# Kernel optimization log

Measured on AMD Instinct MI355X. Metric: run time of the kernel, lower is better.

Reference implementation:

```python
import jax, jax.numpy as jnp
import numpy as np

N = 4096        # batch nodes
E = 65536       # random edges (self-loops appended -> 69632 total)
F_IN = 256
H = 128
C = 2
MIN = 1024      # minority (class 1) count; first MIN nodes
REP = 2         # int(N_pct/100) synthetic reps per minority sample


def setup_inputs() -> dict:
    key = jax.random.key(0)
    ks = jax.random.split(key, 24)
    feat = jax.random.normal(ks[0], (N, F_IN), dtype=jnp.float32)
    src = jax.random.randint(ks[1], (E,), 0, N, dtype=jnp.int32)
    dst = jax.random.randint(ks[2], (E,), 0, N, dtype=jnp.int32)
    loops = jnp.arange(N, dtype=jnp.int32)
    src = jnp.concatenate([src, loops])
    dst = jnp.concatenate([dst, loops])
    # dense batch adjacency (target for EdgeLoss), A[i,j]=1 if edge j->i
    adj = jnp.zeros((N, N), dtype=jnp.float32).at[dst, src].set(1.0)
    # deterministic labels: first MIN nodes are minority class 1
    labels = jnp.concatenate([jnp.ones((MIN,), jnp.int32), jnp.zeros((N - MIN,), jnp.int32)])

    def w(k, shape, fan_in):
        return jax.random.normal(k, shape, dtype=jnp.float32) / np.sqrt(fan_in)

    params = dict(
        W_pool0=w(ks[3], (F_IN, F_IN), F_IN), b_pool0=jnp.zeros((F_IN,), jnp.float32),
        W_self0=w(ks[4], (H, F_IN), F_IN), W_neigh0=w(ks[5], (H, F_IN), F_IN), b0=jnp.zeros((H,), jnp.float32),
        W_pool1=w(ks[6], (H, H), H), b_pool1=jnp.zeros((H,), jnp.float32),
        W_self1=w(ks[7], (H, H), H), W_neigh1=w(ks[8], (H, H), H), b1=jnp.zeros((H,), jnp.float32),
        de_weight=jax.random.uniform(ks[9], (H, H), jnp.float32, -1.0 / np.sqrt(H), 1.0 / np.sqrt(H)),
        W_conv=w(ks[10], (H, 2 * H), 2 * H),
        W_clf=w(ks[11], (C, H), H), b_clf=jnp.zeros((C,), jnp.float32),
        gaps=jax.random.uniform(ks[12], (MIN, REP), jnp.float32),  # SMOTE interpolation gaps
    )
    return dict(feat=feat, adj=adj, src=src, dst=dst, labels=labels, **params)


def _sage_pool_layer(h, src, dst, W_pool, b_pool, W_self, W_neigh, b):
    # DGL SAGEConv aggregator_type='pool': max over neighbors of relu(fc_pool(h))
    p = jax.nn.relu(h @ W_pool.T + b_pool)                     # [N, d]
    hn = jax.ops.segment_max(p[src], dst, num_segments=h.shape[0])
    hn = jnp.where(jnp.isfinite(hn), hn, 0.0)
    return h @ W_self.T + hn @ W_neigh.T + b


def _l2norm(x, eps=1e-12):
    return x / jnp.maximum(jnp.linalg.norm(x, axis=1, keepdims=True), eps)


def _smote_nn_interp(cand, gaps):
    # pairwise euclidean distances (vectorized form of the per-row loop)
    sq = jnp.sum(cand * cand, axis=1)
    d2 = sq[:, None] + sq[None, :] - 2.0 * (cand @ cand.T)
    dist = jnp.sqrt(jnp.maximum(d2, 0.0))
    nn_idx = jnp.argsort(dist, axis=1)[:, 1]                   # k=2 -> single nearest (excl. self)
    diff = cand[nn_idx] - cand                                  # [MIN, H]
    synth = cand[:, None, :] + gaps[:, :, None] * diff[:, None, :]  # [MIN, REP, H], i-major order
    return synth.reshape(MIN * REP, cand.shape[1])


def reference(feat, adj, src, dst, labels,
              W_pool0, b_pool0, W_self0, W_neigh0, b0,
              W_pool1, b_pool1, W_self1, W_neigh1, b1,
              de_weight, W_conv, W_clf, b_clf, gaps):
    # ---- Encoder (2 SAGEConv 'pool' layers; dropout is eval-mode identity) ----
    h = _sage_pool_layer(feat, src, dst, W_pool0, b_pool0, W_self0, W_neigh0, b0)
    h = _l2norm(jax.nn.relu(h))
    h = _sage_pool_layer(h, src, dst, W_pool1, b_pool1, W_self1, W_neigh1, b1)
    # ---- SMOTE (minority = first MIN rows, by deterministic label construction) ----
    synth = _smote_nn_interp(h[:MIN], gaps)
    x = jnp.concatenate([h, synth], axis=0)                    # [N + MIN*REP, H]
    y = jnp.concatenate([labels, jnp.ones((MIN * REP,), jnp.int32)])
    # ---- Decoder: sigmoid(out @ out.T) ----
    out = x @ de_weight.T
    pred_adj = jax.nn.sigmoid(out @ out.T)                     # [6144, 6144]
    # ---- EdgeLoss vs dense batch adjacency ----
    rec = pred_adj[:N, :N]
    edge_num = jnp.sum(adj != 0).astype(jnp.float32)
    neg_w = edge_num / (float(N * N) - edge_num)
    weight = jnp.where(adj == 0, neg_w, 1.0)
    loss = jnp.sum(weight * (rec - adj) ** 2)
    # ---- threshold + SageClassifier (1 layer, no activation before clf) ----
    pred_adj = jnp.where(pred_adj >= 0.5, pred_adj, 0.0)
    neigh = (pred_adj @ x) / (jnp.sum(pred_adj, axis=1, keepdims=True) + 1.0)
    hc = jnp.concatenate([x, neigh], axis=-1) @ W_conv.T
    logits = hc @ W_clf.T + b_clf                              # [6144, 2]
    return logits, y, loss
```

## Files before the change

kernel.cpp:

```cpp
#include <hip/hip_runtime.h>
#include <cstddef>

typedef unsigned short ushort_t;
typedef __attribute__((ext_vector_type(8))) short bf16x8;
typedef __attribute__((ext_vector_type(4))) float f32x4;
typedef __attribute__((ext_vector_type(16))) float f32x16;

#define WS_P0     0u
#define WS_DOTS   0u
#define WS_OBK    524288u
#define WS_HN0    1048576u
#define WS_H1     2097152u
#define WS_H1N    2621440u
#define WS_P1     3145728u
#define WS_PVB    3145728u
#define WS_HN1    3670016u
#define WS_H2     4194304u
#define WS_X      4718592u
#define WS_BITMAP 5767168u
#define WS_NEIGH  6291456u
#define WS_ROWSUM 7077888u
#define WS_SCAL   7084032u
#define WS_DEG    7084048u
#define WS_NN     7088144u
#define WS_CUR    7089168u
#define WS_ROWPTR 7093264u
#define WS_EIDX   7097361u

__device__ inline ushort_t f2bf(float f) {
  unsigned u = __float_as_uint(f);
  u += 0x7fff + ((u >> 16) & 1);
  return (ushort_t)(u >> 16);
}
__device__ inline float bf2f(ushort_t h) {
  return __uint_as_float((unsigned)h << 16);
}

__global__ __launch_bounds__(256, 2) void mgemm(
    const float* __restrict__ A, int lda,
    const float* __restrict__ B, int ldb,
    const float* __restrict__ A2, int lda2,
    const float* __restrict__ B2, int ldb2,
    const float* __restrict__ bias,
    float* __restrict__ C, int ldc,
    int K, int relu,
    ushort_t* __restrict__ Cb,
    const float* __restrict__ a2scale,
    const float* __restrict__ Ahi,
    const float* __restrict__ Wclf,
    const float* __restrict__ scal4,
    float* __restrict__ outp)
{
  __shared__ ushort_t AhS[64][36], AlS[64][36], BhS[64][36], BlS[64][36];
  const int tid = threadIdx.x;
  const int lane = tid & 63;
  const int w = tid >> 6;
  const int lo = lane & 31, hi = lane >> 5;
  const int iq = (w & 1) << 5, jq = (w >> 1) << 5;
  const int i0 = blockIdx.y << 6, j0 = blockIdx.x << 6;
  const int lr = tid >> 2;
  const int c8 = (tid & 3) << 3;
  f32x16 acc;
#pragma unroll
  for (int t = 0; t < 16; ++t) acc[t] = 0.f;
  const int npass = (A2 != nullptr) ? 2 : 1;
  for (int pass = 0; pass < npass; ++pass) {
    const float* Ap = pass ? A2 : A; const int la = pass ? lda2 : lda;
    const float* Bp = pass ? B2 : B; const int lb = pass ? ldb2 : ldb;
    const float* Arow = (pass == 0 && Ahi != nullptr && (i0 + lr) >= 4096)
        ? (Ahi + (size_t)(i0 + lr - 4096) * la)
        : (Ap + (size_t)(i0 + lr) * la);
    const float* Brow = Bp + (size_t)(j0 + lr) * lb;
    const float sc = (pass && a2scale) ? __frcp_rn(a2scale[i0 + lr] + 1.f) : 1.f;
    for (int k0 = 0; k0 < K; k0 += 32) {
      float av[8], bv[8];
      {
        const float4 a0 = *(const float4*)(Arow + k0 + c8);
        const float4 a1 = *(const float4*)(Arow + k0 + c8 + 4);
        const float4 b0 = *(const float4*)(Brow + k0 + c8);
        const float4 b1 = *(const float4*)(Brow + k0 + c8 + 4);
        av[0]=a0.x*sc; av[1]=a0.y*sc; av[2]=a0.z*sc; av[3]=a0.w*sc;
        av[4]=a1.x*sc; av[5]=a1.y*sc; av[6]=a1.z*sc; av[7]=a1.w*sc;
        bv[0]=b0.x; bv[1]=b0.y; bv[2]=b0.z; bv[3]=b0.w;
        bv[4]=b1.x; bv[5]=b1.y; bv[6]=b1.z; bv[7]=b1.w;
      }
      __syncthreads();
      {
        ushort_t ah8[8], al8[8], bh8[8], bl8[8];
#pragma unroll
        for (int e = 0; e < 8; ++e) {
          const ushort_t ah = f2bf(av[e]);
          ah8[e] = ah; al8[e] = f2bf(av[e] - bf2f(ah));
          const ushort_t bh = f2bf(bv[e]);
          bh8[e] = bh; bl8[e] = f2bf(bv[e] - bf2f(bh));
        }
        *(bf16x8*)&AhS[lr][c8] = *(bf16x8*)ah8;
        *(bf16x8*)&AlS[lr][c8] = *(bf16x8*)al8;
        *(bf16x8*)&BhS[lr][c8] = *(bf16x8*)bh8;
        *(bf16x8*)&BlS[lr][c8] = *(bf16x8*)bl8;
      }
      __syncthreads();
#pragma unroll
      for (int kk = 0; kk < 32; kk += 16) {
        const bf16x8 ahf = *(const bf16x8*)&AhS[iq + lo][kk + (hi << 3)];
        const bf16x8 alf = *(const bf16x8*)&AlS[iq + lo][kk + (hi << 3)];
        const bf16x8 bhf = *(const bf16x8*)&BhS[jq + lo][kk + (hi << 3)];
        const bf16x8 blf = *(const bf16x8*)&BlS[jq + lo][kk + (hi << 3)];
        acc = __builtin_amdgcn_mfma_f32_32x32x16_bf16(ahf, bhf, acc, 0, 0, 0);
        acc = __builtin_amdgcn_mfma_f32_32x32x16_bf16(alf, bhf, acc, 0, 0, 0);
        acc = __builtin_amdgcn_mfma_f32_32x32x16_bf16(ahf, blf, acc, 0, 0, 0);
      }
    }
  }
  const int col = j0 + jq + lo;
  if (Wclf) {
    const float w0c = Wclf[col], w1c = Wclf[128 + col];
#pragma unroll
    for (int t = 0; t < 16; ++t) {
      float q0 = acc[t] * w0c, q1 = acc[t] * w1c;
#pragma unroll
      for (int m = 1; m < 32; m <<= 1) {
        q0 += __shfl_xor(q0, m, 64);
        q1 += __shfl_xor(q1, m, 64);
      }
      if (lo == 0) {
        const int row = i0 + iq + (t & 3) + ((t >> 2) << 3) + (hi << 2);
        atomicAdd(&outp[(size_t)row * 2 + 0], q0);
        atomicAdd(&outp[(size_t)row * 2 + 1], q1);
      }
    }
    if (blockIdx.x == 0 && blockIdx.y == 0 && tid == 0) {
      const float cnt = scal4[4];
      const float neg_w = cnt / (16777216.f - cnt);
      outp[18432] = neg_w * (scal4[0] - scal4[3]) + scal4[1];
    }
    return;
  }
  const float badd = bias ? bias[col] : 0.f;
#pragma unroll
  for (int t = 0; t < 16; ++t) {
    float o = acc[t] + badd;
    if (relu) o = fmaxf(o, 0.f);
    const int row = i0 + iq + (t & 3) + ((t >> 2) << 3) + (hi << 2);
    if (Cb) {
      const size_t off = ((size_t)(row >> 5) << 12) +
          (size_t)(((col >> 4) << 9) +
                   (((((col >> 3) & 1) << 5) + (row & 31)) << 3) + (col & 7));
      Cb[off] = f2bf(o);
    } else {
      C[(size_t)row * ldc + col] = o;
    }
  }
}

__global__ void count_bitmap_k(const int* __restrict__ src, const int* __restrict__ dst,
                               int* __restrict__ deg, unsigned* __restrict__ bitmap, int E) {
  const int e = blockIdx.x * 256 + threadIdx.x;
  if (e < E) {
    const int d_ = dst[e], s_ = src[e];
    atomicAdd(&deg[d_], 1);
    const unsigned cell = ((unsigned)d_ << 12) + (unsigned)s_;
    atomicOr(&bitmap[cell >> 5], 1u << (cell & 31));
  }
}

__global__ __launch_bounds__(1024) void scan_k(const int* __restrict__ deg,
                                               int* __restrict__ rowptr,
                                               int* __restrict__ cursor) {
  __shared__ int sums[1024];
  const int t = threadIdx.x;
  const int4 d = *(const int4*)(deg + (t << 2));
  const int local = d.x + d.y + d.z + d.w;
  sums[t] = local;
  __syncthreads();
  for (int off = 1; off < 1024; off <<= 1) {
    int v = (t >= off) ? sums[t - off] : 0;
    __syncthreads();
    sums[t] += v;
    __syncthreads();
  }
  const int excl = sums[t] - local;
  const int o0 = excl, o1 = o0 + d.x, o2 = o1 + d.y, o3 = o2 + d.z;
  rowptr[(t<<2)+0]=o0; rowptr[(t<<2)+1]=o1; rowptr[(t<<2)+2]=o2; rowptr[(t<<2)+3]=o3;
  cursor[(t<<2)+0]=o0; cursor[(t<<2)+1]=o1; cursor[(t<<2)+2]=o2; cursor[(t<<2)+3]=o3;
  if (t == 1023) rowptr[4096] = sums[1023];
}

__global__ void fill_k(const int* __restrict__ src, const int* __restrict__ dst,
                       int* __restrict__ cursor, int* __restrict__ eidx, int E) {
  const int e = blockIdx.x * 256 + threadIdx.x;
  if (e < E) {
    const int p = atomicAdd(&cursor[dst[e]], 1);
    eidx[p] = src[e];
  }
}

__global__ void segmax_k(const float* __restrict__ p, const int* __restrict__ rowptr,
                         const int* __restrict__ eidx, float* __restrict__ hn, int F) {
  const int row = blockIdx.x, f = threadIdx.x;
  const int b = rowptr[row], e = rowptr[row + 1];
  float m0 = 0.f, m1 = 0.f;
  int k = b;
  for (; k + 1 < e; k += 2) {
    m0 = fmaxf(m0, p[(size_t)eidx[k] * F + f]);
    m1 = fmaxf(m1, p[(size_t)eidx[k + 1] * F + f]);
  }
  if (k < e) m0 = fmaxf(m0, p[(size_t)eidx[k] * F + f]);
  hn[(size_t)row * F + f] = fmaxf(m0, m1);
}

__device__ inline float wave_sum(float v) {
#pragma unroll
  for (int o = 32; o > 0; o >>= 1) v += __shfl_down(v, o, 64);
  return v;
}

__global__ void relu_l2norm_k(const float* __restrict__ in, float* __restrict__ out) {
  const int row = blockIdx.x, f = threadIdx.x;
  const float v = fmaxf(in[(size_t)row * 128 + f], 0.f);
  const float ss = wave_sum(v * v);
  __shared__ float w[2];
  if ((f & 63) == 0) w[f >> 6] = ss;
  __syncthreads();
  const float denom = fmaxf(sqrtf(w[0] + w[1]), 1e-12f);
  out[(size_t)row * 128 + f] = v / denom;
}

__global__ void argmin_k(const float* __restrict__ dots, int* __restrict__ nn) {
  __shared__ float sqd[1024];
  const int i = blockIdx.x, tid = threadIdx.x;
#pragma unroll
  for (int z = 0; z < 4; ++z) {
    const int j = (tid << 2) + z;
    sqd[j] = dots[(size_t)j * 1025];
  }
  __syncthreads();
  float best = 3.402823466e38f; int bidx = 0x7fffffff;
  const float si = sqd[i];
  for (int j = tid; j < 1024; j += 256) {
    if (j == i) continue;
    float d2 = si + sqd[j] - 2.f * dots[(size_t)i * 1024 + j];
    d2 = fmaxf(d2, 0.f);
    if (d2 < best || (d2 == best && j < bidx)) { best = d2; bidx = j; }
  }
  __shared__ float bv[256]; __shared__ int bi[256];
  bv[tid] = best; bi[tid] = bidx;
  __syncthreads();
  for (int s = 128; s > 0; s >>= 1) {
    if (tid < s) {
      if (bv[tid+s] < bv[tid] || (bv[tid+s] == bv[tid] && bi[tid+s] < bi[tid])) {
        bv[tid] = bv[tid+s]; bi[tid] = bi[tid+s];
      }
    }
    __syncthreads();
  }
  if (tid == 0) nn[i] = bi[0];
}

__global__ __launch_bounds__(256) void build_pack_k(
    const float* __restrict__ h2, const int* __restrict__ nn,
    const float* __restrict__ gaps, float* __restrict__ synth,
    ushort_t* __restrict__ pvb,
    const int* __restrict__ labels, const float* __restrict__ bclf,
    float* __restrict__ outp) {
  __shared__ ushort_t s[4096];
  const int jt = blockIdx.x, tid = threadIdx.x;
  if (tid < 32) {
    const int i = (jt << 5) + tid;
    outp[(size_t)i * 2 + 0] = bclf[0];
    outp[(size_t)i * 2 + 1] = bclf[1];
    outp[12288 + i] = (i < 4096) ? (float)labels[i] : 1.f;
  }
  if (jt < 128) {
    const float* ip = h2 + ((size_t)jt << 12);
#pragma unroll
    for (int k = 0; k < 4; ++k) {
      const float4 v = *(const float4*)(ip + (tid << 4) + (k << 2));
      ushort4 h; h.x = f2bf(v.x); h.y = f2bf(v.y); h.z = f2bf(v.z); h.w = f2bf(v.w);
      *(ushort4*)(s + (tid << 4) + (k << 2)) = h;
    }
  } else {
    const int row = tid >> 3;
    const int sIdx = ((jt - 128) << 5) + row;
    const int i = sIdx >> 1;
    const float g = gaps[sIdx];
    const int ni = nn[i];
#pragma unroll
    for (int k = 0; k < 4; ++k) {
      const int f = ((tid & 7) << 4) + (k << 2);
      const float4 c4 = *(const float4*)(h2 + (size_t)i * 128 + f);
      const float4 n4 = *(const float4*)(h2 + (size_t)ni * 128 + f);
      float4 v;
      v.x = c4.x + g * (n4.x - c4.x);
      v.y = c4.y + g * (n4.y - c4.y);
      v.z = c4.z + g * (n4.z - c4.z);
      v.w = c4.w + g * (n4.w - c4.w);
      *(float4*)(synth + (size_t)sIdx * 128 + f) = v;
      ushort4 h; h.x = f2bf(v.x); h.y = f2bf(v.y); h.z = f2bf(v.z); h.w = f2bf(v.w);
      *(ushort4*)(s + (row << 7) + f) = h;
    }
  }
  __syncthreads();
  const int u = tid & 31, ft = (tid >> 5) & 3, cc = tid >> 7;
  ushort_t* op = pvb + ((size_t)jt << 12) + (cc << 11) + (ft << 9);
#pragma unroll
  for (int m = 0; m < 2; ++m) {
    const int l = (u << 1) + m;
    const int f = (ft << 5) + (l & 31);
    const int jb = (cc << 4) + ((l >> 5) << 3);
    ushort4 o0, o1;
    o0.x = s[(jb + 0) * 128 + f]; o0.y = s[(jb + 1) * 128 + f];
    o0.z = s[(jb + 2) * 128 + f]; o0.w = s[(jb + 3) * 128 + f];
    o1.x = s[(jb + 4) * 128 + f]; o1.y = s[(jb + 5) * 128 + f];
    o1.z = s[(jb + 6) * 128 + f]; o1.w = s[(jb + 7) * 128 + f];
    *(ushort4*)(op + (l << 3) + 0) = o0;
    *(ushort4*)(op + (l << 3) + 4) = o1;
  }
}

__global__ __launch_bounds__(256, 2) void fused_mfma(
    const ushort_t* __restrict__ obk,
    const ushort_t* __restrict__ pvb,
    const unsigned* __restrict__ bitmap,
    float* __restrict__ neigh,
    float* __restrict__ rowsum,
    float* __restrict__ scal)
{
  __shared__ float wred[4][4];
  const int tid = threadIdx.x;
  const int w = tid >> 6;
  const int lane = tid & 63;
  const int lo = lane & 31, hi = lane >> 5;
  const int it = (blockIdx.x << 2) + w;
  const int iw = it << 5;
  const int jt0 = blockIdx.y * 24;
  const bool loss_i = (it < 128);

  bf16x8 qf[8];
  {
    const ushort_t* qp = obk + ((size_t)it << 12) + (lane << 3);
#pragma unroll
    for (int c = 0; c < 8; ++c) qf[c] = *(const bf16x8*)(qp + (c << 9));
  }
  f32x16 oacc[4];
#pragma unroll
  for (int ft = 0; ft < 4; ++ft)
#pragma unroll
    for (int r = 0; r < 16; ++r) oacc[ft][r] = 0.f;
  float rs = 0.f, s_all = 0.f, s1a = 0.f, suba = 0.f, ecf = 0.f;

  bf16x8 a[8];
  {
    const ushort_t* kp = obk + ((size_t)jt0 << 12) + (lane << 3);
#pragma unroll
    for (int c = 0; c < 8; ++c) a[c] = *(const bf16x8*)(kp + (c << 9));
  }

  for (int t = 0; t < 24; ++t) {
    const int jt = jt0 + t;
    f32x16 s0, s1;
#pragma unroll
    for (int r = 0; r < 16; ++r) { s0[r] = 0.f; s1[r] = 0.f; }
    __builtin_amdgcn_s_setprio(1);
#pragma unroll
    for (int c = 0; c < 4; ++c) {
      s0 = __builtin_amdgcn_mfma_f32_32x32x16_bf16(a[c], qf[c], s0, 0, 0, 0);
      s1 = __builtin_amdgcn_mfma_f32_32x32x16_bf16(a[c + 4], qf[c + 4], s1, 0, 0, 0);
    }
    __builtin_amdgcn_s_setprio(0);
    bf16x8 bvf[2][4];
    {
      const ushort_t* vp = pvb + ((size_t)jt << 12) + (lane << 3);
#pragma unroll
      for (int cc = 0; cc < 2; ++cc)
#pragma unroll
        for (int ft = 0; ft < 4; ++ft)
          bvf[cc][ft] = *(const bf16x8*)(vp + (cc << 11) + (ft << 9));
    }
    if (t < 23) {
      const ushort_t* kp = obk + ((size_t)(jt + 1) << 12) + (lane << 3);
#pragma unroll
      for (int c = 0; c < 8; ++c) a[c] = *(const bf16x8*)(kp + (c << 9));
    }
    const bool loss_t = loss_i && (jt < 128);
    unsigned word = 0u;
    if (loss_t) word = bitmap[((unsigned)(iw + lo) << 7) + (unsigned)jt];
    float p[16];
    if (loss_t) {
      ecf += (float)__popc(word & (0x0F0F0F0Fu << (hi << 2)));
#pragma unroll
      for (int r = 0; r < 16; ++r) {
        const float v = s0[r] + s1[r];
        const float sg = __builtin_amdgcn_rcpf(1.f + __expf(-v));
        const int jl = (r & 3) + ((r >> 2) << 3) + (hi << 2);
        const float e_ = (float)((word >> jl) & 1u);
        s_all += sg * sg;
        s1a  += e_ * (sg - 1.f) * (sg - 1.f);
        suba += e_ * sg * sg;
        const float tv = (v >= 0.f) ? sg : 0.f;
        p[r] = tv; rs += tv;
      }
    } else {
#pragma unroll
      for (int r = 0; r < 16; ++r) {
        const float v = s0[r] + s1[r];
        const float sg = __builtin_amdgcn_rcpf(1.f + __expf(-v));
        const float tv = (v >= 0.f) ? sg : 0.f;
        p[r] = tv; rs += tv;
      }
    }
#pragma unroll
    for (int cc = 0; cc < 2; ++cc) {
      const int b8 = cc << 3;
      unsigned c01, c23, c45, c67;
      asm("v_cvt_pk_bf16_f32 %0, %1, %2" : "=v"(c01) : "v"(p[b8+0]), "v"(p[b8+1]));
      asm("v_cvt_pk_bf16_f32 %0, %1, %2" : "=v"(c23) : "v"(p[b8+2]), "v"(p[b8+3]));
      asm("v_cvt_pk_bf16_f32 %0, %1, %2" : "=v"(c45) : "v"(p[b8+4]), "v"(p[b8+5]));
      asm("v_cvt_pk_bf16_f32 %0, %1, %2" : "=v"(c67) : "v"(p[b8+6]), "v"(p[b8+7]));
      const auto w0 = __builtin_amdgcn_permlane32_swap((int)c01, (int)c45, false, false);
      const auto w1 = __builtin_amdgcn_permlane32_swap((int)c23, (int)c67, false, false);
      union { int i[4]; bf16x8 h; } u;
      u.i[0] = w0[0]; u.i[1] = w1[0]; u.i[2] = w0[1]; u.i[3] = w1[1];
      __builtin_amdgcn_s_setprio(1);
#pragma unroll
      for (int ft = 0; ft < 4; ++ft)
        oacc[ft] = __builtin_amdgcn_mfma_f32_32x32x16_bf16(u.h, bvf[cc][ft], oacc[ft], 0, 0, 0);
      __builtin_amdgcn_s_setprio(0);
    }
  }
#pragma unroll
  for (int ft = 0; ft < 4; ++ft)
#pragma unroll
    for (int r = 0; r < 16; ++r) {
      const int ir = (r & 3) + ((r >> 2) << 3) + (hi << 2);
      atomicAdd(&neigh[(size_t)(iw + ir) * 128 + (ft << 5) + lo], oacc[ft][r]);
    }
  rs += __shfl_xor(rs, 32, 64);
  if (hi == 0) atomicAdd(&rowsum[iw + lo], rs);
  {
    float v0 = wave_sum(s_all), v1 = wave_sum(s1a), v2 = wave_sum(suba), v3 = wave_sum(ecf);
    if (lane == 0) { wred[w][0] = v0; wred[w][1] = v1; wred[w][2] = v2; wred[w][3] = v3; }
  }
  __syncthreads();
  if (tid < 4) {
    const float t = wred[0][tid] + wred[1][tid] + wred[2][tid] + wred[3][tid];
    const int dst = (tid == 0) ? 0 : (tid == 1) ? 1 : (tid == 2) ? 3 : 4;
    atomicAdd(&scal[dst], t);
  }
}

extern "C" void kernel_launch(void* const* d_in, const int* in_sizes, int n_in,
                              void* d_out, int out_size, void* d_ws, size_t ws_size,
                              hipStream_t stream) {
  const float* feat     = (const float*)d_in[0];
  const int*   src      = (const int*)d_in[2];
  const int*   dst      = (const int*)d_in[3];
  const int*   labels   = (const int*)d_in[4];
  const float* W_pool0  = (const float*)d_in[5];
  const float* b_pool0  = (const float*)d_in[6];
  const float* W_self0  = (const float*)d_in[7];
  const float* W_neigh0 = (const float*)d_in[8];
  const float* b0       = (const float*)d_in[9];
  const float* W_pool1  = (const float*)d_in[10];
  const float* b_pool1  = (const float*)d_in[11];
  const float* W_self1  = (const float*)d_in[12];
  const float* W_neigh1 = (const float*)d_in[13];
  const float* b1       = (const float*)d_in[14];
  const float* de_w     = (const float*)d_in[15];
  const float* W_conv   = (const float*)d_in[16];
  const float* W_clf    = (const float*)d_in[17];
  const float* b_clf    = (const float*)d_in[18];
  const float* gaps     = (const float*)d_in[19];
  const int E = in_sizes[2];

  float* ws = (float*)d_ws;
  float* p0       = ws + WS_P0;
  float* dots     = ws + WS_DOTS;
  ushort_t* obk   = (ushort_t*)(ws + WS_OBK);
  float* hn0      = ws + WS_HN0;
  unsigned* bitmap= (unsigned*)(ws + WS_BITMAP);
  float* h1       = ws + WS_H1;
  float* h1n      = ws + WS_H1N;
  float* p1       = ws + WS_P1;
  ushort_t* pvb   = (ushort_t*)(ws + WS_PVB);
  float* hn1      = ws + WS_HN1;
  float* h2       = ws + WS_H2;
  float* synth    = ws + WS_X;
  float* neigh    = ws + WS_NEIGH;
  float* rowsum   = ws + WS_ROWSUM;
  float* scal     = ws + WS_SCAL;
  int* deg        = (int*)(ws + WS_DEG);
  int* nn         = (int*)(ws + WS_NN);
  int* cursor     = (int*)(ws + WS_CUR);
  int* rowptr     = (int*)(ws + WS_ROWPTR);
  int* eidx       = (int*)(ws + WS_EIDX);

  float* outp = (float*)d_out;
  const dim3 blk(256);

  hipMemsetAsync(bitmap, 0, (size_t)(WS_DEG + 4096 - WS_BITMAP) * 4, stream);

  count_bitmap_k<<<(E + 255) / 256, blk, 0, stream>>>(src, dst, deg, bitmap, E);
  scan_k<<<1, 1024, 0, stream>>>(deg, rowptr, cursor);
  fill_k<<<(E + 255) / 256, blk, 0, stream>>>(src, dst, cursor, eidx, E);

  mgemm<<<dim3(4, 64), blk, 0, stream>>>(feat, 256, W_pool0, 256,
                                         nullptr, 0, nullptr, 0,
                                         b_pool0, p0, 256, 256, 1, nullptr, nullptr, nullptr,
                                         nullptr, nullptr, nullptr);
  segmax_k<<<4096, 256, 0, stream>>>(p0, rowptr, eidx, hn0, 256);
  mgemm<<<dim3(2, 64), blk, 0, stream>>>(feat, 256, W_self0, 256,
                                         hn0, 256, W_neigh0, 256,
                                         b0, h1, 128, 256, 0, nullptr, nullptr, nullptr,
                                         nullptr, nullptr, nullptr);
  relu_l2norm_k<<<4096, 128, 0, stream>>>(h1, h1n);

  mgemm<<<dim3(2, 64), blk, 0, stream>>>(h1n, 128, W_pool1, 128,
                                         nullptr, 0, nullptr, 0,
                                         b_pool1, p1, 128, 128, 1, nullptr, nullptr, nullptr,
                                         nullptr, nullptr, nullptr);
  segmax_k<<<4096, 128, 0, stream>>>(p1, rowptr, eidx, hn1, 128);
  mgemm<<<dim3(2, 64), blk, 0, stream>>>(h1n, 128, W_self1, 128,
                                         hn1, 128, W_neigh1, 128,
                                         b1, h2, 128, 128, 0, nullptr, nullptr, nullptr,
                                         nullptr, nullptr, nullptr);

  mgemm<<<dim3(16, 16), blk, 0, stream>>>(h2, 128, h2, 128,
                                          nullptr, 0, nullptr, 0,
                                          nullptr, dots, 1024, 128, 0, nullptr, nullptr, nullptr,
                                          nullptr, nullptr, nullptr);
  argmin_k<<<1024, 256, 0, stream>>>(dots, nn);
  build_pack_k<<<192, blk, 0, stream>>>(h2, nn, gaps, synth, pvb, labels, b_clf, outp);

  mgemm<<<dim3(2, 96), blk, 0, stream>>>(h2, 128, de_w, 128,
                                         nullptr, 0, nullptr, 0,
                                         nullptr, nullptr, 0, 128, 0, obk, nullptr, synth,
                                         nullptr, nullptr, nullptr);
  fused_mfma<<<dim3(48, 8), blk, 0, stream>>>(obk, pvb, bitmap, neigh, rowsum, scal);

  mgemm<<<dim3(2, 96), blk, 0, stream>>>(h2, 128, W_conv, 256,
                                         neigh, 128, W_conv + 128, 256,
                                         nullptr, nullptr, 128, 128, 0, nullptr, rowsum, synth,
                                         W_clf, scal, outp);

  (void)n_in; (void)out_size; (void)ws_size; (void)in_sizes;
}
```

Before: 296.9 us.

## Raise fused_mfma occupancy by splitting j-range and trimming register footprint

Doubles the y-grid of the fused decoder/aggregation kernel so each block covers 12 column tiles instead of 24, and raises the launch-bounds occupancy target from 2 to 3 blocks per CU. Register pressure drops because the next-tile K prefetch is removed, the two split score accumulators become a single chained MFMA accumulator, and the V fragments are loaded per half instead of all at once. The cost is more atomic adds into neigh/rowsum from twice as many blocks, no software prefetch, and a serial dependency chain across the eight score MFMAs.

```diff
diff --git a/kernel.cpp b/kernel.cpp
--- a/kernel.cpp
+++ b/kernel.cpp
@@ -318,7 +318,7 @@
   }
 }
 
-__global__ __launch_bounds__(256, 2) void fused_mfma(
+__global__ __launch_bounds__(256, 3) void fused_mfma(
     const ushort_t* __restrict__ obk,
     const ushort_t* __restrict__ pvb,
     const unsigned* __restrict__ bitmap,
@@ -333,7 +333,7 @@
   const int lo = lane & 31, hi = lane >> 5;
   const int it = (blockIdx.x << 2) + w;
   const int iw = it << 5;
-  const int jt0 = blockIdx.y * 24;
+  const int jt0 = blockIdx.y * 12;
   const bool loss_i = (it < 128);
 
   bf16x8 qf[8];
@@ -349,74 +349,64 @@
     for (int r = 0; r < 16; ++r) oacc[ft][r] = 0.f;
   float rs = 0.f, s_all = 0.f, s1a = 0.f, suba = 0.f, ecf = 0.f;
 
-  bf16x8 a[8];
-  {
-    const ushort_t* kp = obk + ((size_t)jt0 << 12) + (lane << 3);
-#pragma unroll
-    for (int c = 0; c < 8; ++c) a[c] = *(const bf16x8*)(kp + (c << 9));
-  }
-
-  for (int t = 0; t < 24; ++t) {
+  for (int t = 0; t < 12; ++t) {
     const int jt = jt0 + t;
-    f32x16 s0, s1;
-#pragma unroll
-    for (int r = 0; r < 16; ++r) { s0[r] = 0.f; s1[r] = 0.f; }
-    __builtin_amdgcn_s_setprio(1);
-#pragma unroll
-    for (int c = 0; c < 4; ++c) {
-      s0 = __builtin_amdgcn_mfma_f32_32x32x16_bf16(a[c], qf[c], s0, 0, 0, 0);
-      s1 = __builtin_amdgcn_mfma_f32_32x32x16_bf16(a[c + 4], qf[c + 4], s1, 0, 0, 0);
-    }
-    __builtin_amdgcn_s_setprio(0);
-    bf16x8 bvf[2][4];
+    bf16x8 a[8];
     {
-      const ushort_t* vp = pvb + ((size_t)jt << 12) + (lane << 3);
-#pragma unroll
-      for (int cc = 0; cc < 2; ++cc)
-#pragma unroll
-        for (int ft = 0; ft < 4; ++ft)
-          bvf[cc][ft] = *(const bf16x8*)(vp + (cc << 11) + (ft << 9));
-    }
-    if (t < 23) {
-      const ushort_t* kp = obk + ((size_t)(jt + 1) << 12) + (lane << 3);
+      const ushort_t* kp = obk + ((size_t)jt << 12) + (lane << 3);
 #pragma unroll
       for (int c = 0; c < 8; ++c) a[c] = *(const bf16x8*)(kp + (c << 9));
     }
     const bool loss_t = loss_i && (jt < 128);
     unsigned word = 0u;
     if (loss_t) word = bitmap[((unsigned)(iw + lo) << 7) + (unsigned)jt];
-    float p[16];
-    if (loss_t) {
-      ecf += (float)__popc(word & (0x0F0F0F0Fu << (hi << 2)));
-#pragma unroll
-      for (int r = 0; r < 16; ++r) {
-        const float v = s0[r] + s1[r];
-        const float sg = __builtin_amdgcn_rcpf(1.f + __expf(-v));
-        const int jl = (r & 3) + ((r >> 2) << 3) + (hi << 2);
-        const float e_ = (float)((word >> jl) & 1u);
-        s_all += sg * sg;
-        s1a  += e_ * (sg - 1.f) * (sg - 1.f);
-        suba += e_ * sg * sg;
-        const float tv = (v >= 0.f) ? sg : 0.f;
-        p[r] = tv; rs += tv;
-      }
-    } else {
-#pragma unroll
-      for (int r = 0; r < 16; ++r) {
-        const float v = s0[r] + s1[r];
-        const float sg = __builtin_amdgcn_rcpf(1.f + __expf(-v));
-        const float tv = (v >= 0.f) ? sg : 0.f;
-        p[r] = tv; rs += tv;
-      }
-    }
+    f32x16 s;
+#pragma unroll
+    for (int r = 0; r < 16; ++r) s[r] = 0.f;
+    __builtin_amdgcn_s_setprio(1);
+#pragma unroll
+    for (int c = 0; c < 8; ++c)
+      s = __builtin_amdgcn_mfma_f32_32x32x16_bf16(a[c], qf[c], s, 0, 0, 0);
+    __builtin_amdgcn_s_setprio(0);
+    if (loss_t) ecf += (float)__popc(word & (0x0F0F0F0Fu << (hi << 2)));
 #pragma unroll
     for (int cc = 0; cc < 2; ++cc) {
-      const int b8 = cc << 3;
+      bf16x8 bvf[4];
+      {
+        const ushort_t* vp = pvb + ((size_t)jt << 12) + (cc << 11) + (lane << 3);
+#pragma unroll
+        for (int ft = 0; ft < 4; ++ft)
+          bvf[ft] = *(const bf16x8*)(vp + (ft << 9));
+      }
+      float p8[8];
+      if (loss_t) {
+#pragma unroll
+        for (int rr = 0; rr < 8; ++rr) {
+          const int r = (cc << 3) + rr;
+          const float v = s[r];
+          const float sg = __builtin_amdgcn_rcpf(1.f + __expf(-v));
+          const int jl = (r & 3) + ((r >> 2) << 3) + (hi << 2);
+          const float e_ = (float)((word >> jl) & 1u);
+          s_all += sg * sg;
+          s1a  += e_ * (sg - 1.f) * (sg - 1.f);
+          suba += e_ * sg * sg;
+          const float tv = (v >= 0.f) ? sg : 0.f;
+          p8[rr] = tv; rs += tv;
+        }
+      } else {
+#pragma unroll
+        for (int rr = 0; rr < 8; ++rr) {
+          const float v = s[(cc << 3) + rr];
+          const float sg = __builtin_amdgcn_rcpf(1.f + __expf(-v));
+          const float tv = (v >= 0.f) ? sg : 0.f;
+          p8[rr] = tv; rs += tv;
+        }
+      }
       unsigned c01, c23, c45, c67;
-      asm("v_cvt_pk_bf16_f32 %0, %1, %2" : "=v"(c01) : "v"(p[b8+0]), "v"(p[b8+1]));
-      asm("v_cvt_pk_bf16_f32 %0, %1, %2" : "=v"(c23) : "v"(p[b8+2]), "v"(p[b8+3]));
-      asm("v_cvt_pk_bf16_f32 %0, %1, %2" : "=v"(c45) : "v"(p[b8+4]), "v"(p[b8+5]));
-      asm("v_cvt_pk_bf16_f32 %0, %1, %2" : "=v"(c67) : "v"(p[b8+6]), "v"(p[b8+7]));
+      asm("v_cvt_pk_bf16_f32 %0, %1, %2" : "=v"(c01) : "v"(p8[0]), "v"(p8[1]));
+      asm("v_cvt_pk_bf16_f32 %0, %1, %2" : "=v"(c23) : "v"(p8[2]), "v"(p8[3]));
+      asm("v_cvt_pk_bf16_f32 %0, %1, %2" : "=v"(c45) : "v"(p8[4]), "v"(p8[5]));
+      asm("v_cvt_pk_bf16_f32 %0, %1, %2" : "=v"(c67) : "v"(p8[6]), "v"(p8[7]));
       const auto w0 = __builtin_amdgcn_permlane32_swap((int)c01, (int)c45, false, false);
       const auto w1 = __builtin_amdgcn_permlane32_swap((int)c23, (int)c67, false, false);
       union { int i[4]; bf16x8 h; } u;
@@ -424,7 +414,7 @@
       __builtin_amdgcn_s_setprio(1);
 #pragma unroll
       for (int ft = 0; ft < 4; ++ft)
-        oacc[ft] = __builtin_amdgcn_mfma_f32_32x32x16_bf16(u.h, bvf[cc][ft], oacc[ft], 0, 0, 0);
+        oacc[ft] = __builtin_amdgcn_mfma_f32_32x32x16_bf16(u.h, bvf[ft], oacc[ft], 0, 0, 0);
       __builtin_amdgcn_s_setprio(0);
     }
   }
@@ -536,7 +526,7 @@
                                          nullptr, 0, nullptr, 0,
                                          nullptr, nullptr, 0, 128, 0, obk, nullptr, synth,
                                          nullptr, nullptr, nullptr);
-  fused_mfma<<<dim3(48, 8), blk, 0, stream>>>(obk, pvb, bitmap, neigh, rowsum, scal);
+  fused_mfma<<<dim3(48, 16), blk, 0, stream>>>(obk, pvb, bitmap, neigh, rowsum, scal);
 
   mgemm<<<dim3(2, 96), blk, 0, stream>>>(h2, 128, W_conv, 256,
                                          neigh, 128, W_conv + 128, 256,
```

Result: slower. 324.0 us (+9.1%).
